# Performance work log

Measured on AMD Instinct MI355X. Metric: run time of the kernel, lower is better.

## Reference

```python
import jax, jax.numpy as jnp
import numpy as np

# Device / mapping constants from the source (is_low_resistance=True branch)
V_REF = 0.25
G_MIN = 0.1
G_MAX = 1.0
K_V = 2.0 * V_REF  # x_to_V scale
N_AVG = 2.18
N_STD = 0.115


def setup_inputs() -> dict:
    key = jax.random.key(0)
    k_x, k_wp, k_wn, k_n = jax.random.split(key, 4)
    n_in, n_out, batch = 1024, 512, 128
    stdv = 1.0 / np.sqrt(n_in)
    x = jax.random.uniform(k_x, (batch, n_in), dtype=jnp.float32)
    w_pos = 0.5 + stdv * jax.random.normal(k_wp, (n_in, n_out), dtype=jnp.float32)
    w_neg = 0.5 + stdv * jax.random.normal(k_wn, (n_in, n_out), dtype=jnp.float32)
    b_pos = 0.5 * jnp.ones((n_out,), jnp.float32)
    b_neg = 0.5 * jnp.ones((n_out,), jnp.float32)
    # per-device I-V nonlinearity parameter n ~ N(n_avg, n_std), one per crossbar cell
    n_param = N_AVG + N_STD * jax.random.normal(k_n, (n_in + 1, 2 * n_out), dtype=jnp.float32)
    return {"x": x, "w_pos": w_pos, "w_neg": w_neg, "b_pos": b_pos, "b_neg": b_neg,
            "n_param": n_param}


def _memristor_dense(x, w_pos, w_neg, b_pos, b_neg, n_param):
    x = jnp.clip(x, 0.0, 1.0)
    # append bias rows, interleave pos/neg along output axis -> (n_in+1, 2*n_out)
    cw_pos = jnp.concatenate([w_pos, b_pos[None, :]], axis=0)
    cw_neg = jnp.concatenate([w_neg, b_neg[None, :]], axis=0)
    w = jnp.stack([cw_pos, cw_neg], axis=-1).reshape(cw_pos.shape[0], -1)
    # append ones column to inputs (bias voltage line)
    inp = jnp.concatenate([x, jnp.ones((x.shape[0], 1), x.dtype)], axis=1)  # (B, n_in+1)
    # weight -> effective conductance (differential scheme), then offset by G_min
    max_w = jnp.max(jnp.abs(w))
    k_G = (G_MAX - G_MIN) / max_w
    G = jnp.abs(k_G * w) + G_MIN  # (n_in+1, 2*n_out)
    # input -> voltage
    V = K_V * inp  # (B, n_in+1)
    # nonlinear-parameter I-V model: I = sign(V) * G * V_ref * (|V|/V_ref) ** (log2(n) + 1)
    # (satisfies n = I(2*V_ref) / (2 * I(V_ref)))
    exponent = jnp.log2(n_param) + 1.0  # (n_in+1, 2*n_out)
    v_ratio = jnp.abs(V) / V_REF  # (B, n_in+1)
    vr = v_ratio[:, :, None]  # (B, n_in+1, 1)
    vr_safe = jnp.where(vr > 0, vr, 1.0)
    pow_term = jnp.where(vr > 0, vr_safe ** exponent[None, :, :], 0.0)  # (B, n_in+1, 2*n_out)
    I_ind = jnp.sign(V)[:, :, None] * (G * V_REF)[None, :, :] * pow_term
    # sum currents along bit lines
    I = jnp.sum(I_ind, axis=1)  # (B, 2*n_out)
    # currents -> outputs (differential pairs are interleaved)
    y = (I[:, 0::2] - I[:, 1::2]) / (K_V * k_G)  # (B, n_out)
    return y


def reference(x, w_pos, w_neg, b_pos, b_neg, n_param):
    return _memristor_dense(x, w_pos, w_neg, b_pos, b_neg, n_param)
```

## Files before the change

### kernel.cpp

```cpp
#include <hip/hip_runtime.h>
#include <hip/hip_bf16.h>


#define LOG2F(v)  __builtin_amdgcn_logf(v)
#define EXP2F(v)  __builtin_amdgcn_exp2f(v)

#define NJ 16
#define NB 32
#define KI 64
#define KROW4 65
#define LROW 68

#define NPART 256

__global__ __launch_bounds__(256) void setup1_kernel(
    const float* __restrict__ w_pos, const float* __restrict__ w_neg,
    const float* __restrict__ b_pos, const float* __restrict__ b_neg,
    float* __restrict__ ws) {
  const int t = threadIdx.x, blk = blockIdx.x;
  const float4* wp4 = (const float4*)w_pos;
  const float4* wn4 = (const float4*)w_neg;
  float m = 0.0f;
  #pragma unroll
  for (int r = 0; r < 2; ++r) {
    int i = blk * 512 + r * 256 + t;
    float4 a = wp4[i], b = wn4[i];
    m = fmaxf(m, fmaxf(fmaxf(fabsf(a.x), fabsf(a.y)), fmaxf(fabsf(a.z), fabsf(a.w))));
    m = fmaxf(m, fmaxf(fmaxf(fabsf(b.x), fabsf(b.y)), fmaxf(fabsf(b.z), fabsf(b.w))));
  }
  if (blk == 0) {
    m = fmaxf(m, fmaxf(fabsf(b_pos[t]), fabsf(b_pos[t + 256])));
    m = fmaxf(m, fmaxf(fabsf(b_neg[t]), fabsf(b_neg[t + 256])));
  }
  #pragma unroll
  for (int off = 32; off > 0; off >>= 1)
    m = fmaxf(m, __shfl_down(m, off, 64));
  __shared__ float sm[4];
  int lane = t & 63, wv = t >> 6;
  if (lane == 0) sm[wv] = m;
  __syncthreads();
  if (t == 0)
    ws[blk] = fmaxf(fmaxf(sm[0], sm[1]), fmaxf(sm[2], sm[3]));
}

__global__ __launch_bounds__(512) void memristor_kernel(
    const float* __restrict__ x, const float* __restrict__ w_pos,
    const float* __restrict__ w_neg, const float* __restrict__ b_pos,
    const float* __restrict__ b_neg, const float* __restrict__ n_param,
    const float* __restrict__ ws, float* __restrict__ y) {
  __shared__ float4 sP[NJ * KROW4];
  __shared__ float  sL[NB * LROW];

  const float4* mp4 = (const float4*)ws;
  float4 m4 = mp4[0];
  #pragma unroll 16
  for (int i = 1; i < NPART / 4; ++i) {
    float4 v = mp4[i];
    m4.x = fmaxf(m4.x, v.x); m4.y = fmaxf(m4.y, v.y);
    m4.z = fmaxf(m4.z, v.z); m4.w = fmaxf(m4.w, v.w);
  }
  const float mw = fmaxf(fmaxf(m4.x, m4.y), fmaxf(m4.z, m4.w));
  const float c0 = mw * (0.05f / 0.9f);

  const int j0 = blockIdx.x * NJ;
  const int b0 = blockIdx.y * NB;
  const int zt = blockIdx.z;
  const int t  = threadIdx.x;
  const int jj = t & 15;
  const int bb = t >> 4;
  float accP = 0.0f, accN = 0.0f;

  const float2* np2 = (const float2*)n_param;

  for (int c = 0; c < 4; ++c) {
    const int i0 = zt * 256 + c * KI;
    #pragma unroll
    for (int r = 0; r < (NB * KI) / 512; ++r) {
      int idx = r * 512 + t;
      int k  = idx & (KI - 1);
      int bl = idx >> 6;
      float v = x[(b0 + bl) * 1024 + i0 + k];
      v = fminf(fmaxf(v, 0.0f), 1.0f);
      sL[bl * LROW + k] = LOG2F(2.0f * v);
    }
    #pragma unroll
    for (int r = 0; r < (NJ * KI) / 512; ++r) {
      int idx = r * 512 + t;
      int jl = idx & (NJ - 1);
      int il = idx >> 4;
      int gi = i0 + il;
      float wp = w_pos[gi * 512 + j0 + jl];
      float wn = w_neg[gi * 512 + j0 + jl];
      float2 np = np2[gi * 512 + j0 + jl];
      sP[jl * KROW4 + il] = make_float4(
          fmaf(0.5f, fabsf(wp), c0), LOG2F(np.x) + 1.0f,
          fmaf(0.5f, fabsf(wn), c0), LOG2F(np.y) + 1.0f);
    }
    __syncthreads();
    const float4* pP = &sP[jj * KROW4];
    const float*  pL = &sL[bb * LROW];
    #pragma unroll 8
    for (int k = 0; k < KI; ++k) {
      float4 p = pP[k];
      float l  = pL[k];
      accP = fmaf(p.x, EXP2F(p.y * l), accP);
      accN = fmaf(p.z, EXP2F(p.w * l), accN);
    }
    __syncthreads();
  }

  if (zt == 3) {
    int jg = j0 + jj;
    float2 np = np2[1024 * 512 + jg];
    float a0 = fmaf(0.5f, fabsf(b_pos[jg]), c0);
    float a1 = fmaf(0.5f, fabsf(b_neg[jg]), c0);
    accP = fmaf(a0, EXP2F(LOG2F(np.x) + 1.0f), accP);
    accN = fmaf(a1, EXP2F(LOG2F(np.y) + 1.0f), accN);
  }

  atomicAdd(&y[(b0 + bb) * 512 + (j0 + jj)], accP - accN);
}

__global__ __launch_bounds__(256) void zero_y_kernel(float4* __restrict__ y4) {
  y4[blockIdx.x * 256 + threadIdx.x] = make_float4(0.f, 0.f, 0.f, 0.f);
}

extern "C" void kernel_launch(void* const* d_in, const int* in_sizes, int n_in,
                              void* d_out, int out_size, void* d_ws, size_t ws_size,
                              hipStream_t stream) {
  const float* x       = (const float*)d_in[0];
  const float* w_pos   = (const float*)d_in[1];
  const float* w_neg   = (const float*)d_in[2];
  const float* b_pos   = (const float*)d_in[3];
  const float* b_neg   = (const float*)d_in[4];
  const float* n_param = (const float*)d_in[5];
  float* y   = (float*)d_out;
  float* wsf = (float*)d_ws;

  (void)hipMemsetAsync(d_out, 0, (size_t)out_size * 4, stream);

  setup1_kernel<<<dim3(NPART), dim3(256), 0, stream>>>(
      w_pos, w_neg, b_pos, b_neg, wsf);

  memristor_kernel<<<dim3(32, 4, 4), dim3(512), 0, stream>>>(
      x, w_pos, w_neg, b_pos, b_neg, n_param, wsf, y);
}
```

Measured before the change: 95.63 us.

## Drop split-K and memset, prefetch tiles into registers, atomicMax weight reduction

The main kernel no longer splits the reduction dimension across blockIdx.z. Each block now covers all of K in 16 chunks with 256 threads. The next chunk's weights, n_param and x are prefetched into registers while the current chunk is computed from shared memory. Outputs are stored directly, which removes the output memset and the atomicAdds. The setup kernel reduces max|w| with one atomicMax into the workspace instead of writing per-block partials that were re-reduced in the main kernel. In exchange, each thread has a longer serial loop, there are fewer waves overall, and the atomicMax depends on the workspace never being reset holding a value no larger than the true max.

```diff
diff --git a/kernel.cpp b/kernel.cpp
--- a/kernel.cpp
+++ b/kernel.cpp
@@ -6,17 +6,16 @@
 #define EXP2F(v)  __builtin_amdgcn_exp2f(v)
 
 #define NJ 16
-#define NB 32
+#define NB 16
 #define KI 64
+#define NCH 16
 #define KROW4 65
 #define LROW 68
-
-#define NPART 256
 
 __global__ __launch_bounds__(256) void setup1_kernel(
     const float* __restrict__ w_pos, const float* __restrict__ w_neg,
     const float* __restrict__ b_pos, const float* __restrict__ b_neg,
-    float* __restrict__ ws) {
+    int* __restrict__ ws) {
   const int t = threadIdx.x, blk = blockIdx.x;
   const float4* wp4 = (const float4*)w_pos;
   const float4* wn4 = (const float4*)w_neg;
@@ -39,11 +38,13 @@
   int lane = t & 63, wv = t >> 6;
   if (lane == 0) sm[wv] = m;
   __syncthreads();
-  if (t == 0)
-    ws[blk] = fmaxf(fmaxf(sm[0], sm[1]), fmaxf(sm[2], sm[3]));
+  if (t == 0) {
+    m = fmaxf(fmaxf(sm[0], sm[1]), fmaxf(sm[2], sm[3]));
+    atomicMax(ws, __float_as_int(m));
+  }
 }
 
-__global__ __launch_bounds__(512) void memristor_kernel(
+__global__ __launch_bounds__(256) void memristor_kernel(
     const float* __restrict__ x, const float* __restrict__ w_pos,
     const float* __restrict__ w_neg, const float* __restrict__ b_pos,
     const float* __restrict__ b_neg, const float* __restrict__ n_param,
@@ -51,52 +52,57 @@
   __shared__ float4 sP[NJ * KROW4];
   __shared__ float  sL[NB * LROW];
 
-  const float4* mp4 = (const float4*)ws;
-  float4 m4 = mp4[0];
-  #pragma unroll 16
-  for (int i = 1; i < NPART / 4; ++i) {
-    float4 v = mp4[i];
-    m4.x = fmaxf(m4.x, v.x); m4.y = fmaxf(m4.y, v.y);
-    m4.z = fmaxf(m4.z, v.z); m4.w = fmaxf(m4.w, v.w);
-  }
-  const float mw = fmaxf(fmaxf(m4.x, m4.y), fmaxf(m4.z, m4.w));
+  const float mw = ws[0];
   const float c0 = mw * (0.05f / 0.9f);
 
   const int j0 = blockIdx.x * NJ;
   const int b0 = blockIdx.y * NB;
-  const int zt = blockIdx.z;
   const int t  = threadIdx.x;
   const int jj = t & 15;
   const int bb = t >> 4;
+
+  const int s_jl = t & 15;
+  const int s_il = t >> 4;
+  const int s_k  = t & 63;
+  const int s_bl = t >> 6;
+
+  const float2* np2 = (const float2*)n_param;
+  float wpR[4], wnR[4], xR[4];
+  float2 npR[4];
+
+  #pragma unroll
+  for (int r = 0; r < 4; ++r) {
+    int gi = s_il + r * 16;
+    wpR[r] = w_pos[gi * 512 + j0 + s_jl];
+    wnR[r] = w_neg[gi * 512 + j0 + s_jl];
+    npR[r] = np2[gi * 512 + j0 + s_jl];
+    xR[r]  = x[(b0 + s_bl + r * 4) * 1024 + s_k];
+  }
+
   float accP = 0.0f, accN = 0.0f;
 
-  const float2* np2 = (const float2*)n_param;
-
-  for (int c = 0; c < 4; ++c) {
-    const int i0 = zt * 256 + c * KI;
+  for (int c = 0; c < NCH; ++c) {
     #pragma unroll
-    for (int r = 0; r < (NB * KI) / 512; ++r) {
-      int idx = r * 512 + t;
-      int k  = idx & (KI - 1);
-      int bl = idx >> 6;
-      float v = x[(b0 + bl) * 1024 + i0 + k];
-      v = fminf(fmaxf(v, 0.0f), 1.0f);
-      sL[bl * LROW + k] = LOG2F(2.0f * v);
-    }
-    #pragma unroll
-    for (int r = 0; r < (NJ * KI) / 512; ++r) {
-      int idx = r * 512 + t;
-      int jl = idx & (NJ - 1);
-      int il = idx >> 4;
-      int gi = i0 + il;
-      float wp = w_pos[gi * 512 + j0 + jl];
-      float wn = w_neg[gi * 512 + j0 + jl];
-      float2 np = np2[gi * 512 + j0 + jl];
-      sP[jl * KROW4 + il] = make_float4(
-          fmaf(0.5f, fabsf(wp), c0), LOG2F(np.x) + 1.0f,
-          fmaf(0.5f, fabsf(wn), c0), LOG2F(np.y) + 1.0f);
+    for (int r = 0; r < 4; ++r) {
+      int il = s_il + r * 16;
+      sP[s_jl * KROW4 + il] = make_float4(
+          fmaf(0.5f, fabsf(wpR[r]), c0), LOG2F(npR[r].x) + 1.0f,
+          fmaf(0.5f, fabsf(wnR[r]), c0), LOG2F(npR[r].y) + 1.0f);
+      float v = fminf(fmaxf(xR[r], 0.0f), 1.0f);
+      sL[(s_bl + r * 4) * LROW + s_k] = LOG2F(2.0f * v);
     }
     __syncthreads();
+    if (c < NCH - 1) {
+      const int i0 = (c + 1) * KI;
+      #pragma unroll
+      for (int r = 0; r < 4; ++r) {
+        int gi = i0 + s_il + r * 16;
+        wpR[r] = w_pos[gi * 512 + j0 + s_jl];
+        wnR[r] = w_neg[gi * 512 + j0 + s_jl];
+        npR[r] = np2[gi * 512 + j0 + s_jl];
+        xR[r]  = x[(b0 + s_bl + r * 4) * 1024 + i0 + s_k];
+      }
+    }
     const float4* pP = &sP[jj * KROW4];
     const float*  pL = &sL[bb * LROW];
     #pragma unroll 8
@@ -109,7 +115,7 @@
     __syncthreads();
   }
 
-  if (zt == 3) {
+  {
     int jg = j0 + jj;
     float2 np = np2[1024 * 512 + jg];
     float a0 = fmaf(0.5f, fabsf(b_pos[jg]), c0);
@@ -118,11 +124,7 @@
     accN = fmaf(a1, EXP2F(LOG2F(np.y) + 1.0f), accN);
   }
 
-  atomicAdd(&y[(b0 + bb) * 512 + (j0 + jj)], accP - accN);
-}
-
-__global__ __launch_bounds__(256) void zero_y_kernel(float4* __restrict__ y4) {
-  y4[blockIdx.x * 256 + threadIdx.x] = make_float4(0.f, 0.f, 0.f, 0.f);
+  y[(b0 + bb) * 512 + (j0 + jj)] = accP - accN;
 }
 
 extern "C" void kernel_launch(void* const* d_in, const int* in_sizes, int n_in,
@@ -135,13 +137,10 @@
   const float* b_neg   = (const float*)d_in[4];
   const float* n_param = (const float*)d_in[5];
   float* y   = (float*)d_out;
-  float* wsf = (float*)d_ws;
 
-  (void)hipMemsetAsync(d_out, 0, (size_t)out_size * 4, stream);
+  setup1_kernel<<<dim3(256), dim3(256), 0, stream>>>(
+      w_pos, w_neg, b_pos, b_neg, (int*)d_ws);
 
-  setup1_kernel<<<dim3(NPART), dim3(256), 0, stream>>>(
-      w_pos, w_neg, b_pos, b_neg, wsf);
-
-  memristor_kernel<<<dim3(32, 4, 4), dim3(512), 0, stream>>>(
-      x, w_pos, w_neg, b_pos, b_neg, n_param, wsf, y);
+  memristor_kernel<<<dim3(32, 8), dim3(256), 0, stream>>>(
+      x, w_pos, w_neg, b_pos, b_neg, n_param, (const float*)d_ws, y);
 }
```

New measurement: 107.7 us. +12.6%, slower.
